# Performance work log

Measured on AMD Instinct MI355X. Metric: run time of the kernel, lower is better.

## Reference

```python
import jax, jax.numpy as jnp
import numpy as np

MATRIX_SIZE = 64  # m; chol params T = m*(m+1)//2 = 2080
INPUT_SIZE = 512
BATCH = 8192


def setup_inputs() -> dict:
    key = jax.random.key(0)
    k1, k2, k3 = jax.random.split(key, 3)
    T = MATRIX_SIZE * (MATRIX_SIZE + 1) // 2
    x = jax.random.normal(k1, (BATCH, INPUT_SIZE), dtype=jnp.float32)
    # nn.Linear params: W [T, input_size], b [T]
    W = jax.random.normal(k2, (T, INPUT_SIZE), dtype=jnp.float32) / np.sqrt(INPUT_SIZE)
    b = jax.random.normal(k3, (T,), dtype=jnp.float32) * 0.01
    return {"x": x, "W": W, "b": b}


def reference(x, W, b):
    m = MATRIX_SIZE
    # fc: [B, T] Cholesky parameters
    chol = x @ W.T + b
    # Row-major lower-triangle ordering (i, j<=i) matches the original idx loop
    rows, cols = np.tril_indices(m)           # each [T]
    diag = jnp.asarray(rows == cols)           # [T] bool
    # ReLU on diagonal entries, identity off-diagonal (single fused where)
    vals = jnp.where(diag[None, :], jax.nn.relu(chol), chol)  # [B, T]
    B = x.shape[0]
    L = jnp.zeros((B, m, m), dtype=chol.dtype).at[:, rows, cols].set(vals)
    # L @ L^T per batch element -> positive semidefinite [B, m, m]
    return jnp.einsum('bij,bkj->bik', L, L)
```

## Files before the change

kernel.cpp:

```cpp
#include <hip/hip_runtime.h>
#include <stdint.h>

#define MDIM 8192
#define KDIM 512
#define TDIM 2080
#define NPAD 2176
#define MSZ  64

typedef __attribute__((ext_vector_type(8))) __bf16 bf16x8;
typedef __attribute__((ext_vector_type(4))) float  f32x4;

__device__ __forceinline__ unsigned short f2bf(float f) {
    unsigned int u = __float_as_uint(f);
    u += 0x7fffu + ((u >> 16) & 1u);
    return (unsigned short)(u >> 16);
}

#define NX4 (MDIM * KDIM / 4)
#define NW4 (NPAD * KDIM / 4)

__global__ __launch_bounds__(256) void convert_kernel(const float* __restrict__ x,
                                                      const float* __restrict__ W,
                                                      unsigned short* __restrict__ xb,
                                                      unsigned short* __restrict__ wb) {
    int idx = blockIdx.x * 256 + threadIdx.x;
    if (idx < NX4) {
        float4 v = reinterpret_cast<const float4*>(x)[idx];
        reinterpret_cast<ushort4*>(xb)[idx] =
            make_ushort4(f2bf(v.x), f2bf(v.y), f2bf(v.z), f2bf(v.w));
    } else {
        int j = idx - NX4;
        if (j >= NW4) return;
        int n = (j * 4) >> 9;
        ushort4 o = make_ushort4(0, 0, 0, 0);
        if (n < TDIM) {
            float4 v = reinterpret_cast<const float4*>(W)[j];
            o = make_ushort4(f2bf(v.x), f2bf(v.y), f2bf(v.z), f2bf(v.w));
        }
        reinterpret_cast<ushort4*>(wb)[j] = o;
    }
}

typedef __attribute__((address_space(1))) void as1_void;
typedef __attribute__((address_space(3))) void as3_void;

__device__ __forceinline__ void gload_lds16(const void* g, void* l) {
    __builtin_amdgcn_global_load_lds((as1_void*)(void*)g, (as3_void*)l, 16, 0, 0);
}

__device__ __forceinline__ bf16x8 frag_load(const unsigned short* base, int row, int kbyte) {
    kbyte ^= (row & 7) << 4;
    return *reinterpret_cast<const bf16x8*>(reinterpret_cast<const char*>(base) + row * 128 + kbyte);
}

__device__ __forceinline__ int tril_row(int n) {
    int i = (int)((sqrtf((float)(8 * n + 1)) - 1.0f) * 0.5f);
    while ((i + 1) * (i + 2) / 2 <= n) ++i;
    while (i * (i + 1) / 2 > n) --i;
    return i;
}

__global__ __launch_bounds__(256) void gemm_kernel(const unsigned short* __restrict__ xb,
                                                   const unsigned short* __restrict__ wb,
                                                   const float* __restrict__ bias,
                                                   unsigned short* __restrict__ chol) {
    __shared__ __align__(16) unsigned short As[128 * 64];
    __shared__ __align__(16) unsigned short Bs[128 * 64];
    const int tid  = threadIdx.x;
    const int lane = tid & 63;
    const int wave = tid >> 6;
    const int m0 = blockIdx.y * 128;
    const int n0 = blockIdx.x * 128;
    const int wm = (wave >> 1) * 64;
    const int wn = (wave & 1) * 64;
    const int lr = lane & 15;
    const int lq = lane >> 4;

    f32x4 acc[4][4];
    f32x4 zero = {0.f, 0.f, 0.f, 0.f};
#pragma unroll
    for (int i = 0; i < 4; ++i)
#pragma unroll
        for (int j = 0; j < 4; ++j) acc[i][j] = zero;

    for (int k0 = 0; k0 < KDIM; k0 += 64) {
        const unsigned short* ga = xb + (size_t)m0 * KDIM + k0;
        const unsigned short* gb = wb + (size_t)n0 * KDIM + k0;
#pragma unroll
        for (int c = 0; c < 4; ++c) {
            int flat = c * 256 + tid;
            int row  = flat >> 3;
            int ch   = (flat & 7) ^ (row & 7);
            unsigned short* lb = (unsigned short*)As + (size_t)(c * 256 + (tid & 192)) * 8;
            gload_lds16(ga + row * KDIM + ch * 8, lb);
        }
#pragma unroll
        for (int c = 0; c < 4; ++c) {
            int flat = c * 256 + tid;
            int row  = flat >> 3;
            int ch   = (flat & 7) ^ (row & 7);
            unsigned short* lb = (unsigned short*)Bs + (size_t)(c * 256 + (tid & 192)) * 8;
            gload_lds16(gb + row * KDIM + ch * 8, lb);
        }
        __syncthreads();
#pragma unroll
        for (int kk = 0; kk < 2; ++kk) {
            bf16x8 af[4], bf[4];
            int kb = kk * 64 + lq * 16;
#pragma unroll
            for (int i = 0; i < 4; ++i) {
                af[i] = frag_load(As, wm + i * 16 + lr, kb);
                bf[i] = frag_load(Bs, wn + i * 16 + lr, kb);
            }
#pragma unroll
            for (int mi = 0; mi < 4; ++mi)
#pragma unroll
                for (int ni = 0; ni < 4; ++ni)
                    acc[mi][ni] = __builtin_amdgcn_mfma_f32_16x16x32_bf16(af[mi], bf[ni], acc[mi][ni], 0, 0, 0);
        }
        __syncthreads();
    }

#pragma unroll
    for (int ni = 0; ni < 4; ++ni) {
        int n = n0 + wn + ni * 16 + lr;
        float bv = 0.f;
        bool isdiag = false;
        if (n < TDIM) {
            bv = bias[n];
            int i = tril_row(n);
            isdiag = (n - i * (i + 1) / 2 == i);
        }
#pragma unroll
        for (int mi = 0; mi < 4; ++mi) {
#pragma unroll
            for (int r = 0; r < 4; ++r) {
                int m = m0 + wm + mi * 16 + lq * 4 + r;
                float v = acc[mi][ni][r] + bv;
                if (isdiag && v < 0.f) v = 0.f;
                chol[(size_t)m * NPAD + n] = f2bf(v);
            }
        }
    }
}

__device__ __forceinline__ void lds_store_swz(unsigned short* L, int i, int j, unsigned short v) {
    int ch   = ((j >> 3) ^ i) & 7;
    int addr = i * 128 + (ch << 4) + ((j & 7) * 2);
    *reinterpret_cast<unsigned short*>(reinterpret_cast<char*>(L) + addr) = v;
}

__global__ __launch_bounds__(256) void syrk_kernel(const unsigned short* __restrict__ chol,
                                                   float* __restrict__ out) {
    __shared__ __align__(16) unsigned short Ls[4][64 * 64];
    const int tid  = threadIdx.x;
    const int lane = tid & 63;
    const int wave = tid >> 6;
    const int batch = blockIdx.x * 4 + wave;
    unsigned short* L = Ls[wave];

    const unsigned int* row = reinterpret_cast<const unsigned int*>(chol + (size_t)batch * NPAD);
    unsigned int vals[17];
#pragma unroll
    for (int c = 0; c < 17; ++c) {
        int t = lane + c * 64;
        vals[c] = (t < TDIM / 2) ? row[t] : 0u;
    }

#pragma unroll
    for (int c = 0; c < 8; ++c)
        *reinterpret_cast<int4*>(reinterpret_cast<char*>(L) + (c * 64 + lane) * 16) = make_int4(0, 0, 0, 0);
    __builtin_amdgcn_sched_barrier(0);

#pragma unroll
    for (int c = 0; c < 17; ++c) {
        int t = lane + c * 64;
        if (t < TDIM / 2) {
            unsigned int v = vals[c];
            int n = 2 * t;
            int i = tril_row(n);
            int j = n - i * (i + 1) / 2;
            lds_store_swz(L, i, j, (unsigned short)(v & 0xffffu));
            int i2 = i, j2 = j + 1;
            if (j2 > i2) { i2 = i + 1; j2 = 0; }
            lds_store_swz(L, i2, j2, (unsigned short)(v >> 16));
        }
    }
    asm volatile("s_waitcnt lgkmcnt(0)" ::: "memory");
    __builtin_amdgcn_sched_barrier(0);

    const int lr = lane & 15;
    const int lq = lane >> 4;
    bf16x8 fr[4][2];
#pragma unroll
    for (int i = 0; i < 4; ++i)
#pragma unroll
        for (int kk = 0; kk < 2; ++kk)
            fr[i][kk] = frag_load(L, i * 16 + lr, kk * 64 + lq * 16);

    f32x4 acc[4][4];
    f32x4 zero = {0.f, 0.f, 0.f, 0.f};
#pragma unroll
    for (int i = 0; i < 4; ++i)
#pragma unroll
        for (int j = 0; j < 4; ++j) acc[i][j] = zero;

#pragma unroll
    for (int mi = 0; mi < 4; ++mi)
#pragma unroll
        for (int ni = 0; ni < 4; ++ni)
#pragma unroll
            for (int kk = 0; kk < 2; ++kk)
                acc[mi][ni] = __builtin_amdgcn_mfma_f32_16x16x32_bf16(fr[mi][kk], fr[ni][kk], acc[mi][ni], 0, 0, 0);

    float* ob = out + (size_t)batch * (MSZ * MSZ);
#pragma unroll
    for (int mi = 0; mi < 4; ++mi)
#pragma unroll
        for (int ni = 0; ni < 4; ++ni)
            *reinterpret_cast<f32x4*>(ob + (ni * 16 + lr) * MSZ + mi * 16 + lq * 4) = acc[mi][ni];
}

extern "C" void kernel_launch(void* const* d_in, const int* in_sizes, int n_in,
                              void* d_out, int out_size, void* d_ws, size_t ws_size,
                              hipStream_t stream) {
    (void)in_sizes; (void)n_in; (void)out_size; (void)ws_size;
    const float* x = (const float*)d_in[0];
    const float* W = (const float*)d_in[1];
    const float* b = (const float*)d_in[2];
    float* out = (float*)d_out;

    unsigned short* xb   = (unsigned short*)d_ws;
    unsigned short* wb   = xb + (size_t)MDIM * KDIM;
    unsigned short* chol = wb + (size_t)NPAD * KDIM;

    int conv_blocks = (NX4 + NW4 + 255) / 256;
    convert_kernel<<<dim3(conv_blocks), dim3(256), 0, stream>>>(x, W, xb, wb);
    gemm_kernel<<<dim3(NPAD / 128, MDIM / 128), dim3(256), 0, stream>>>(xb, wb, b, chol);
    syrk_kernel<<<dim3(MDIM / 4), dim3(256), 0, stream>>>(chol, out);
}
```

Baseline: 81.91 us.

## Vectorize GEMM epilogue stores, precompute bias/diag mask, remap blocks per XCD

Swaps the MFMA operands so each lane holds four consecutive n columns, which lets the GEMM epilogue write ushort4 vectors instead of scattered 2-byte stores. Bias and a diagonal mask are precomputed once in the convert kernel, so the epilogue no longer evaluates the triangular-row sqrt loop per column. GEMM and SYRK block indices are remapped so neighbouring tiles and batches land on the same XCD, aiming for better L2 locality. This adds a small extra workspace buffer and slightly more work in the convert kernel.

```diff
diff --git a/kernel.cpp b/kernel.cpp
--- a/kernel.cpp
+++ b/kernel.cpp
@@ -16,21 +16,31 @@
     return (unsigned short)(u >> 16);
 }
 
+__device__ __forceinline__ int tril_row(int n) {
+    int i = (int)((sqrtf((float)(8 * n + 1)) - 1.0f) * 0.5f);
+    while ((i + 1) * (i + 2) / 2 <= n) ++i;
+    while (i * (i + 1) / 2 > n) --i;
+    return i;
+}
+
 #define NX4 (MDIM * KDIM / 4)
 #define NW4 (NPAD * KDIM / 4)
+#define NT4 (NPAD / 4)
 
 __global__ __launch_bounds__(256) void convert_kernel(const float* __restrict__ x,
                                                       const float* __restrict__ W,
+                                                      const float* __restrict__ b,
                                                       unsigned short* __restrict__ xb,
-                                                      unsigned short* __restrict__ wb) {
+                                                      unsigned short* __restrict__ wb,
+                                                      float* __restrict__ biasf,
+                                                      float* __restrict__ diagm) {
     int idx = blockIdx.x * 256 + threadIdx.x;
     if (idx < NX4) {
         float4 v = reinterpret_cast<const float4*>(x)[idx];
         reinterpret_cast<ushort4*>(xb)[idx] =
             make_ushort4(f2bf(v.x), f2bf(v.y), f2bf(v.z), f2bf(v.w));
-    } else {
+    } else if (idx < NX4 + NW4) {
         int j = idx - NX4;
-        if (j >= NW4) return;
         int n = (j * 4) >> 9;
         ushort4 o = make_ushort4(0, 0, 0, 0);
         if (n < TDIM) {
@@ -38,6 +48,22 @@
             o = make_ushort4(f2bf(v.x), f2bf(v.y), f2bf(v.z), f2bf(v.w));
         }
         reinterpret_cast<ushort4*>(wb)[j] = o;
+    } else {
+        int t = idx - NX4 - NW4;
+        if (t < NT4) {
+#pragma unroll
+            for (int r = 0; r < 4; ++r) {
+                int n = t * 4 + r;
+                float bv = 0.f, dm = 0.f;
+                if (n < TDIM) {
+                    bv = b[n];
+                    int i = tril_row(n);
+                    dm = (n - i * (i + 1) / 2 == i) ? 1.f : 0.f;
+                }
+                biasf[n] = bv;
+                diagm[n] = dm;
+            }
+        }
     }
 }
 
@@ -53,24 +79,25 @@
     return *reinterpret_cast<const bf16x8*>(reinterpret_cast<const char*>(base) + row * 128 + kbyte);
 }
 
-__device__ __forceinline__ int tril_row(int n) {
-    int i = (int)((sqrtf((float)(8 * n + 1)) - 1.0f) * 0.5f);
-    while ((i + 1) * (i + 2) / 2 <= n) ++i;
-    while (i * (i + 1) / 2 > n) --i;
-    return i;
-}
-
 __global__ __launch_bounds__(256) void gemm_kernel(const unsigned short* __restrict__ xb,
                                                    const unsigned short* __restrict__ wb,
-                                                   const float* __restrict__ bias,
+                                                   const float* __restrict__ biasf,
+                                                   const float* __restrict__ diagm,
                                                    unsigned short* __restrict__ chol) {
     __shared__ __align__(16) unsigned short As[128 * 64];
     __shared__ __align__(16) unsigned short Bs[128 * 64];
     const int tid  = threadIdx.x;
     const int lane = tid & 63;
     const int wave = tid >> 6;
-    const int m0 = blockIdx.y * 128;
-    const int n0 = blockIdx.x * 128;
+
+    const int bid = blockIdx.x;
+    const int xcd = bid & 7;
+    const int c   = bid >> 3;
+    const int mt  = xcd * 8 + c / 17;
+    const int nt  = c % 17;
+    const int m0 = mt * 128;
+    const int n0 = nt * 128;
+
     const int wm = (wave >> 1) * 64;
     const int wn = (wave & 1) * 64;
     const int lr = lane & 15;
@@ -87,19 +114,19 @@
         const unsigned short* ga = xb + (size_t)m0 * KDIM + k0;
         const unsigned short* gb = wb + (size_t)n0 * KDIM + k0;
 #pragma unroll
-        for (int c = 0; c < 4; ++c) {
-            int flat = c * 256 + tid;
+        for (int cc = 0; cc < 4; ++cc) {
+            int flat = cc * 256 + tid;
             int row  = flat >> 3;
             int ch   = (flat & 7) ^ (row & 7);
-            unsigned short* lb = (unsigned short*)As + (size_t)(c * 256 + (tid & 192)) * 8;
+            unsigned short* lb = (unsigned short*)As + (size_t)(cc * 256 + (tid & 192)) * 8;
             gload_lds16(ga + row * KDIM + ch * 8, lb);
         }
 #pragma unroll
-        for (int c = 0; c < 4; ++c) {
-            int flat = c * 256 + tid;
+        for (int cc = 0; cc < 4; ++cc) {
+            int flat = cc * 256 + tid;
             int row  = flat >> 3;
             int ch   = (flat & 7) ^ (row & 7);
-            unsigned short* lb = (unsigned short*)Bs + (size_t)(c * 256 + (tid & 192)) * 8;
+            unsigned short* lb = (unsigned short*)Bs + (size_t)(cc * 256 + (tid & 192)) * 8;
             gload_lds16(gb + row * KDIM + ch * 8, lb);
         }
         __syncthreads();
@@ -116,30 +143,27 @@
             for (int mi = 0; mi < 4; ++mi)
 #pragma unroll
                 for (int ni = 0; ni < 4; ++ni)
-                    acc[mi][ni] = __builtin_amdgcn_mfma_f32_16x16x32_bf16(af[mi], bf[ni], acc[mi][ni], 0, 0, 0);
+                    acc[mi][ni] = __builtin_amdgcn_mfma_f32_16x16x32_bf16(bf[ni], af[mi], acc[mi][ni], 0, 0, 0);
         }
         __syncthreads();
     }
 
+    const float4* bt = reinterpret_cast<const float4*>(biasf);
+    const float4* dt = reinterpret_cast<const float4*>(diagm);
 #pragma unroll
     for (int ni = 0; ni < 4; ++ni) {
-        int n = n0 + wn + ni * 16 + lr;
-        float bv = 0.f;
-        bool isdiag = false;
-        if (n < TDIM) {
-            bv = bias[n];
-            int i = tril_row(n);
-            isdiag = (n - i * (i + 1) / 2 == i);
-        }
+        int nb = n0 + wn + ni * 16 + lq * 4;
+        float4 bv = bt[nb >> 2];
+        float4 dm = dt[nb >> 2];
 #pragma unroll
         for (int mi = 0; mi < 4; ++mi) {
-#pragma unroll
-            for (int r = 0; r < 4; ++r) {
-                int m = m0 + wm + mi * 16 + lq * 4 + r;
-                float v = acc[mi][ni][r] + bv;
-                if (isdiag && v < 0.f) v = 0.f;
-                chol[(size_t)m * NPAD + n] = f2bf(v);
-            }
+            int m = m0 + wm + mi * 16 + lr;
+            float v0 = acc[mi][ni][0] + bv.x; if (dm.x != 0.f && v0 < 0.f) v0 = 0.f;
+            float v1 = acc[mi][ni][1] + bv.y; if (dm.y != 0.f && v1 < 0.f) v1 = 0.f;
+            float v2 = acc[mi][ni][2] + bv.z; if (dm.z != 0.f && v2 < 0.f) v2 = 0.f;
+            float v3 = acc[mi][ni][3] + bv.w; if (dm.w != 0.f && v3 < 0.f) v3 = 0.f;
+            *reinterpret_cast<ushort4*>(&chol[(size_t)m * NPAD + nb]) =
+                make_ushort4(f2bf(v0), f2bf(v1), f2bf(v2), f2bf(v3));
         }
     }
 }
@@ -156,7 +180,10 @@
     const int tid  = threadIdx.x;
     const int lane = tid & 63;
     const int wave = tid >> 6;
-    const int batch = blockIdx.x * 4 + wave;
+
+    const int bid = blockIdx.x;
+    const int bb  = (bid & 7) * 256 + (bid >> 3);
+    const int batch = bb * 4 + wave;
     unsigned short* L = Ls[wave];
 
     const unsigned int* row = reinterpret_cast<const unsigned int*>(chol + (size_t)batch * NPAD);
@@ -233,9 +260,11 @@
     unsigned short* xb   = (unsigned short*)d_ws;
     unsigned short* wb   = xb + (size_t)MDIM * KDIM;
     unsigned short* chol = wb + (size_t)NPAD * KDIM;
-
-    int conv_blocks = (NX4 + NW4 + 255) / 256;
-    convert_kernel<<<dim3(conv_blocks), dim3(256), 0, stream>>>(x, W, xb, wb);
-    gemm_kernel<<<dim3(NPAD / 128, MDIM / 128), dim3(256), 0, stream>>>(xb, wb, b, chol);
+    float* biasf = (float*)(chol + (size_t)MDIM * NPAD);
+    float* diagm = biasf + NPAD;
+
+    int conv_blocks = (NX4 + NW4 + NT4 + 255) / 256;
+    convert_kernel<<<dim3(conv_blocks), dim3(256), 0, stream>>>(x, W, b, xb, wb, biasf, diagm);
+    gemm_kernel<<<dim3(17 * 64), dim3(256), 0, stream>>>(xb, wb, biasf, diagm, chol);
     syrk_kernel<<<dim3(MDIM / 4), dim3(256), 0, stream>>>(chol, out);
 }
```

Measured after the change: 74.05 us. -9.6%, faster.
